# Performance work log

Hardware: AMD Instinct MI355X
Metric: run time of the kernel (lower is better)

## Reference

```python
import jax, jax.numpy as jnp
import numpy as np

N_NODES = 100000
D_IN = 128
D_OUT = 128
SHAPES = {"r1": 1, "r2": 2, "r3": 3}
N_EDGES = {"r1": 400000, "r2": 300000, "r3": 200000}


def setup_inputs() -> dict:
    key = jax.random.key(0)
    ks = jax.random.split(key, 10)
    inp = {
        "x": jax.random.normal(ks[0], (N_NODES, D_IN), dtype=jnp.float32),
        "A_r1": jax.random.normal(ks[1], (D_IN * 1, D_OUT), dtype=jnp.float32) * 0.05,
        "A_r2": jax.random.normal(ks[2], (D_IN * 2, D_OUT), dtype=jnp.float32) * 0.05,
        "A_r3": jax.random.normal(ks[3], (D_IN * 3, D_OUT), dtype=jnp.float32) * 0.05,
        "C_w": jax.random.normal(ks[4], (D_IN, D_OUT), dtype=jnp.float32) * 0.05,
        "C_b": jax.random.normal(ks[5], (D_OUT,), dtype=jnp.float32) * 0.05,
    }
    for j, (name, shape) in enumerate(SHAPES.items()):
        n = N_EDGES[name] * shape
        inp[f"ei_{name}"] = jax.random.randint(ks[6 + j], (2, n), 0, N_NODES, dtype=jnp.int64)
    return inp


def _edge_type_agg(x, edge_indices, A, shape):
    # edge_indices: [2, n_edges*shape]; row0 = sources, row1 reshaped -> dest per hyperedge
    dest = edge_indices[1].reshape(-1, shape)[:, 0]          # [n_edges]
    gathered = x[edge_indices[0]].reshape(-1, shape * x.shape[1])  # [n_edges, shape*D_IN]
    msg = gathered @ A                                        # [n_edges, D_OUT]
    # 1/count(dest) normalization (torch.unique counts == per-type in-degree)
    deg = jax.ops.segment_sum(jnp.ones_like(dest, dtype=msg.dtype), dest, num_segments=x.shape[0])
    msg = msg / deg[dest][:, None]
    return jax.ops.segment_sum(msg, dest, num_segments=x.shape[0])  # scatter_add


def reference(x, ei_r1, ei_r2, ei_r3, A_r1, A_r2, A_r3, C_w, C_b):
    agg = (_edge_type_agg(x, ei_r1, A_r1, 1)
           + _edge_type_agg(x, ei_r2, A_r2, 2)
           + _edge_type_agg(x, ei_r3, A_r3, 3))
    return x @ C_w + C_b + agg
```

## Files before the change

### kernel.cpp

```cpp
#include <hip/hip_runtime.h>

#define N_NODES 100000
#define D 128

typedef unsigned short u16;
typedef short s16x8 __attribute__((ext_vector_type(8)));
typedef float f32x4 __attribute__((ext_vector_type(4)));
typedef unsigned u32x4 __attribute__((ext_vector_type(4)));


#define ENTS_OFF 2804224L
#define AT_OFF   9204224L
#define XB_OFF   9433600L
#define G_OFF    35033600L

__device__ __forceinline__ u16 f2b(float f) {
    union { float f; unsigned u; } v; v.f = f;
    unsigned r = (v.u + 0x7FFFu + ((v.u >> 16) & 1u)) >> 16;
    return (u16)r;
}
__device__ __forceinline__ unsigned pk(float lo, float hi) {
    return (unsigned)f2b(lo) | ((unsigned)f2b(hi) << 16);
}
__device__ __forceinline__ float blo(unsigned w) { return __uint_as_float(w << 16); }
__device__ __forceinline__ float bhi(unsigned w) { return __uint_as_float(w & 0xFFFF0000u); }


__global__ __launch_bounds__(256) void deg_all(
    const int* __restrict__ e1, const int* __restrict__ e2, const int* __restrict__ e3,
    int ne1, int ne2, int ne3, int* __restrict__ deg) {
    int g = blockIdx.x * 256 + threadIdx.x;
    if (g < ne1) {
        atomicAdd(&deg[e1[ne1 + g]], 1);
    } else if (g < ne1 + ne2) {
        int e = g - ne1;
        atomicAdd(&deg[N_NODES + e2[ne2 * 2 + e * 2]], 1);
    } else if (g < ne1 + ne2 + ne3) {
        int e = g - ne1 - ne2;
        atomicAdd(&deg[2 * N_NODES + e3[ne3 * 3 + e * 3]], 1);
    }
}


__global__ __launch_bounds__(256) void scan_atb(
    const int* __restrict__ deg, int* __restrict__ offs, int* __restrict__ cursor,
    int* __restrict__ flags,
    const float* __restrict__ A1, const float* __restrict__ A2,
    const float* __restrict__ A3, const float* __restrict__ Cw,
    u16* __restrict__ ATb, int n, int nb) {
    const int t = threadIdx.x, bid = blockIdx.x;
    if (bid >= nb) {
        int mb = bid - nb;
        int m = mb >> 6;
        int idx = (mb & 63) * 256 + t;
        int nn = idx >> 7, kk = idx & 127;
        const float* src; int srow;
        if (m == 0)      { src = A1; srow = kk; }
        else if (m < 3)  { src = A2; srow = (m - 1) * 128 + kk; }
        else if (m < 6)  { src = A3; srow = (m - 3) * 128 + kk; }
        else             { src = Cw; srow = kk; }
        ATb[m * 16384 + nn * 128 + kk] = f2b(src[(long)srow * 128 + nn]);
        return;
    }
    __shared__ int s[256];
    __shared__ int bprefix;
    int base = bid * 1024 + t * 4;
    int d1[4], d2[4], v[4], p[4];
#pragma unroll
    for (int r = 0; r < 4; r++) {
        int idx = base + r;
        if (idx < n) {
            d1[r] = deg[idx];
            d2[r] = deg[N_NODES + idx];
            int d3 = deg[2 * N_NODES + idx];
            v[r] = d1[r] + 2 * d2[r] + 3 * d3;
        } else { d1[r] = 0; d2[r] = 0; v[r] = 0; }
    }
    p[0] = 0; p[1] = v[0]; p[2] = v[0] + v[1]; p[3] = v[0] + v[1] + v[2];
    int tsum = p[3] + v[3];
    s[t] = tsum;
    for (int off = 1; off < 256; off <<= 1) {
        __syncthreads();
        int x = (t >= off) ? s[t - off] : 0;
        __syncthreads();
        s[t] += x;
    }
    __syncthreads();
    int total = s[255];
    if (t == 0) {
        int run = 0;
        if (bid == 0) {
            atomicExch(&flags[0], (total << 2) | 2);
        } else {
            atomicExch(&flags[bid], (total << 2) | 1);
            int j = bid - 1;
            while (true) {
                int f = atomicAdd(&flags[j], 0);
                int st = f & 3;
                if (st == 0) continue;
                run += (f >> 2);
                if (st == 2) break;
                j--;
            }
            atomicExch(&flags[bid], ((run + total) << 2) | 2);
        }
        bprefix = run;
        if (bid == nb - 1) offs[n] = run + total;
    }
    __syncthreads();
    int texcl = s[t] - tsum + bprefix;
#pragma unroll
    for (int r = 0; r < 4; r++) {
        int idx = base + r;
        if (idx < n) {
            int val = texcl + p[r];
            offs[idx] = val;
            cursor[idx] = val;
            cursor[N_NODES + idx] = val + d1[r];
            cursor[2 * N_NODES + idx] = val + d1[r] + 2 * d2[r];
        }
    }
}


__global__ __launch_bounds__(256) void scatter_xconv(
    const float* __restrict__ x, u16* __restrict__ xb,
    const int* __restrict__ e1, const int* __restrict__ e2, const int* __restrict__ e3,
    int ne1, int ne2, int ne3, const int* __restrict__ deg,
    int* __restrict__ cursor, int* __restrict__ ents) {
    int b = blockIdx.x, t = threadIdx.x;
    if (b < 6250) {
        int f = b * 256 + t;
        int node = f >> 4, j = f & 15;
        const f32x4* xr = (const f32x4*)(x + (long)node * 128 + j * 8);
        f32x4 v0 = __builtin_nontemporal_load(xr);
        f32x4 v1 = __builtin_nontemporal_load(xr + 1);
        u32x4 o;
        o.x = pk(v0.x, v0.y); o.y = pk(v0.z, v0.w);
        o.z = pk(v1.x, v1.y); o.w = pk(v1.z, v1.w);
        *(u32x4*)(xb + (long)node * 128 + j * 8) = o;
        return;
    }
    int g = (b - 6250) * 256 + t;
    if (g < ne1) {
        int dest = e1[ne1 + g];
        int pos = atomicAdd(&cursor[dest], 1);
        ents[pos] = e1[g];
    } else if (g < ne1 + ne2) {
        int e = g - ne1;
        int dest = e2[ne2 * 2 + e * 2];
        int c2 = deg[N_NODES + dest];
        int pos = atomicAdd(&cursor[N_NODES + dest], 1);
        ents[pos]      = e2[e * 2];
        ents[pos + c2] = e2[e * 2 + 1];
    } else if (g < ne1 + ne2 + ne3) {
        int e = g - ne1 - ne2;
        int dest = e3[ne3 * 3 + e * 3];
        int c3 = deg[2 * N_NODES + dest];
        int pos = atomicAdd(&cursor[2 * N_NODES + dest], 1);
        ents[pos]          = e3[e * 3];
        ents[pos + c3]     = e3[e * 3 + 1];
        ents[pos + 2 * c3] = e3[e * 3 + 2];
    }
}


__global__ __launch_bounds__(256) void agg_all(
    const u16* __restrict__ xb, const int* __restrict__ ents,
    const int* __restrict__ offs, const int* __restrict__ deg,
    u16* __restrict__ G) {
    const int lane = threadIdx.x & 63;
    const int wv = __builtin_amdgcn_readfirstlane(threadIdx.x >> 6);
    int wid = blockIdx.x * 4 + wv;
    const int nw = gridDim.x * 4;
    const unsigned cb = (unsigned)lane * 4u;
    const char* xbb = (const char*)xb;

    for (int d = wid; d < N_NODES; d += nw) {
        const int lo = offs[d];
        const int c1 = deg[d], c2 = deg[N_NODES + d], c3 = deg[2 * N_NODES + d];
        float a0l = 0, a0h = 0, a1l = 0, a1h = 0, a2l = 0, a2h = 0;
        float a3l = 0, a3h = 0, a4l = 0, a4h = 0, a5l = 0, a5h = 0;

        int p = 0;
        for (; p + 8 <= c1; p += 8) {
            unsigned w[8];
#pragma unroll
            for (int i = 0; i < 8; i++)
                w[i] = *(const unsigned*)(xbb + (((unsigned)ents[lo + p + i] << 8) + cb));
#pragma unroll
            for (int i = 0; i < 8; i++) { a0l += blo(w[i]); a0h += bhi(w[i]); }
        }
        for (; p < c1; p++) {
            unsigned w = *(const unsigned*)(xbb + (((unsigned)ents[lo + p] << 8) + cb));
            a0l += blo(w); a0h += bhi(w);
        }

        const int o1 = lo + c1;
        p = 0;
        for (; p + 4 <= c2; p += 4) {
            unsigned wa[4], wb[4];
#pragma unroll
            for (int i = 0; i < 4; i++) {
                int e = o1 + p + i;
                wa[i] = *(const unsigned*)(xbb + (((unsigned)ents[e] << 8) + cb));
                wb[i] = *(const unsigned*)(xbb + (((unsigned)ents[e + c2] << 8) + cb));
            }
#pragma unroll
            for (int i = 0; i < 4; i++) {
                a1l += blo(wa[i]); a1h += bhi(wa[i]);
                a2l += blo(wb[i]); a2h += bhi(wb[i]);
            }
        }
        for (; p < c2; p++) {
            int e = o1 + p;
            unsigned wa = *(const unsigned*)(xbb + (((unsigned)ents[e] << 8) + cb));
            unsigned wb = *(const unsigned*)(xbb + (((unsigned)ents[e + c2] << 8) + cb));
            a1l += blo(wa); a1h += bhi(wa);
            a2l += blo(wb); a2h += bhi(wb);
        }

        const int o3 = o1 + 2 * c2;
        p = 0;
        for (; p + 4 <= c3; p += 4) {
            unsigned wa[4], wb[4], wc[4];
#pragma unroll
            for (int i = 0; i < 4; i++) {
                int e = o3 + p + i;
                wa[i] = *(const unsigned*)(xbb + (((unsigned)ents[e] << 8) + cb));
                wb[i] = *(const unsigned*)(xbb + (((unsigned)ents[e + c3] << 8) + cb));
                wc[i] = *(const unsigned*)(xbb + (((unsigned)ents[e + 2 * c3] << 8) + cb));
            }
#pragma unroll
            for (int i = 0; i < 4; i++) {
                a3l += blo(wa[i]); a3h += bhi(wa[i]);
                a4l += blo(wb[i]); a4h += bhi(wb[i]);
                a5l += blo(wc[i]); a5h += bhi(wc[i]);
            }
        }
        for (; p < c3; p++) {
            int e = o3 + p;
            unsigned wa = *(const unsigned*)(xbb + (((unsigned)ents[e] << 8) + cb));
            unsigned wb = *(const unsigned*)(xbb + (((unsigned)ents[e + c3] << 8) + cb));
            unsigned wc = *(const unsigned*)(xbb + (((unsigned)ents[e + 2 * c3] << 8) + cb));
            a3l += blo(wa); a3h += bhi(wa);
            a4l += blo(wb); a4h += bhi(wb);
            a5l += blo(wc); a5h += bhi(wc);
        }

        const float i1 = c1 ? 1.0f / (float)c1 : 0.0f;
        const float i2 = c2 ? 1.0f / (float)c2 : 0.0f;
        const float i3 = c3 ? 1.0f / (float)c3 : 0.0f;
        char* gd = (char*)G + (size_t)d * 1536 + cb;
        __builtin_nontemporal_store(pk(a0l * i1, a0h * i1), (unsigned*)gd);
        __builtin_nontemporal_store(pk(a1l * i2, a1h * i2), (unsigned*)(gd + 256));
        __builtin_nontemporal_store(pk(a2l * i2, a2h * i2), (unsigned*)(gd + 512));
        __builtin_nontemporal_store(pk(a3l * i3, a3h * i3), (unsigned*)(gd + 768));
        __builtin_nontemporal_store(pk(a4l * i3, a4h * i3), (unsigned*)(gd + 1024));
        __builtin_nontemporal_store(pk(a5l * i3, a5h * i3), (unsigned*)(gd + 1280));
    }
}


__global__ __launch_bounds__(256) void gemm_out(
    const u16* __restrict__ G, const u16* __restrict__ xb,
    const u16* __restrict__ AT, const float* __restrict__ Cb,
    float* __restrict__ out) {
    __shared__ __align__(16) u16 Xs[2][4][64][40];

    const int t = threadIdx.x;
    const int d0 = blockIdx.x * 64;
    const int lane = t & 63, wv = t >> 6;
    const int nbase = wv * 32, quad = lane >> 4, lrow = lane & 15;

    f32x4 acc[4][2];
#pragma unroll
    for (int mi = 0; mi < 4; mi++)
#pragma unroll
        for (int ni = 0; ni < 2; ni++) acc[mi][ni] = (f32x4)(0.0f);

    u32x4 stg[4];
#pragma unroll
    for (int i = 0; i < 4; i++) {
        int f = i * 256 + t;
        int row = f >> 4, k8 = f & 15;
        long rs = (d0 + row < N_NODES) ? d0 + row : N_NODES - 1;
        stg[i] = __builtin_nontemporal_load((const u32x4*)(G + rs * 768 + k8 * 8));
    }
#pragma unroll
    for (int i = 0; i < 4; i++) {
        int f = i * 256 + t;
        int row = f >> 4, k8 = f & 15;
        *(u32x4*)&Xs[0][k8 >> 2][row][(k8 & 3) * 8] = stg[i];
    }
    __syncthreads();

    for (int s = 0; s < 7; s++) {
        if (s < 6) {
#pragma unroll
            for (int i = 0; i < 4; i++) {
                int f = i * 256 + t;
                int row = f >> 4, k8 = f & 15;
                long rs = (d0 + row < N_NODES) ? d0 + row : N_NODES - 1;
                const u16* src = (s + 1 < 6) ? (G + rs * 768 + (s + 1) * 128 + k8 * 8)
                                             : (xb + rs * 128 + k8 * 8);
                stg[i] = __builtin_nontemporal_load((const u32x4*)src);
            }
        }
        const u16* B = AT + s * 16384;
        s16x8 bfrag[2][4];
#pragma unroll
        for (int ni = 0; ni < 2; ni++)
#pragma unroll
            for (int c = 0; c < 4; c++)
                bfrag[ni][c] = *(const s16x8*)(B + (nbase + ni * 16 + lrow) * 128 +
                                               c * 32 + quad * 8);
        const int cur = s & 1;
#pragma unroll
        for (int c = 0; c < 4; c++) {
            s16x8 a[4];
#pragma unroll
            for (int mi = 0; mi < 4; mi++)
                a[mi] = *(const s16x8*)&Xs[cur][c][mi * 16 + lrow][quad * 8];
#pragma unroll
            for (int mi = 0; mi < 4; mi++)
#pragma unroll
                for (int ni = 0; ni < 2; ni++)
                    acc[mi][ni] = __builtin_amdgcn_mfma_f32_16x16x32_bf16(
                        a[mi], bfrag[ni][c], acc[mi][ni], 0, 0, 0);
        }
        if (s < 6) {
#pragma unroll
            for (int i = 0; i < 4; i++) {
                int f = i * 256 + t;
                int row = f >> 4, k8 = f & 15;
                *(u32x4*)&Xs[cur ^ 1][k8 >> 2][row][(k8 & 3) * 8] = stg[i];
            }
        }
        __syncthreads();
    }

    float* smf = (float*)&Xs[0][0][0][0];
#pragma unroll
    for (int mi = 0; mi < 4; mi++)
#pragma unroll
        for (int ni = 0; ni < 2; ni++)
#pragma unroll
            for (int reg = 0; reg < 4; reg++) {
                int row = mi * 16 + quad * 4 + reg;
                int colq = nbase + ni * 16 + lrow;
                smf[row * 132 + colq] = acc[mi][ni][reg];
            }
    __syncthreads();
#pragma unroll
    for (int i = 0; i < 8; i++) {
        int f = i * 256 + t;
        int row = f >> 5;
        int colq = (f & 31) * 4;
        if (d0 + row < N_NODES) {
            f32x4 v = *(const f32x4*)&smf[row * 132 + colq];
            f32x4 b = *(const f32x4*)&Cb[colq];
            v += b;
            __builtin_nontemporal_store(v, (f32x4*)&out[(long)(d0 + row) * 128 + colq]);
        }
    }
}


extern "C" void kernel_launch(void* const* d_in, const int* in_sizes, int n_in,
                              void* d_out, int out_size, void* d_ws, size_t ws_size,
                              hipStream_t stream) {
    const float* x  = (const float*)d_in[0];
    const float* A1 = (const float*)d_in[1];
    const float* A2 = (const float*)d_in[2];
    const float* A3 = (const float*)d_in[3];
    const float* Cw = (const float*)d_in[4];
    const float* Cb = (const float*)d_in[5];
    const int* e1 = (const int*)d_in[6];
    const int* e2 = (const int*)d_in[7];
    const int* e3 = (const int*)d_in[8];
    float* out = (float*)d_out;

    int* ws = (int*)d_ws;
    int* deg    = ws;
    int* flags  = ws + 300000;
    int* offs   = ws + 300128;
    int* cursor = ws + 400129;
    int* ents   = (int*)((char*)d_ws + ENTS_OFF);
    u16* ATb    = (u16*)((char*)d_ws + AT_OFF);
    u16* xb     = (u16*)((char*)d_ws + XB_OFF);
    u16* G      = (u16*)((char*)d_ws + G_OFF);

    const int NE1 = in_sizes[6] / 2;
    const int NE2 = in_sizes[7] / (2 * 2);
    const int NE3 = in_sizes[8] / (2 * 3);
    const int NET = NE1 + NE2 + NE3;
    const int n = N_NODES;
    const int NB = (n + 1023) / 1024;

    hipMemsetAsync(deg, 0, (300000 + 128) * sizeof(int), stream);
    deg_all<<<(NET + 255) / 256, 256, 0, stream>>>(e1, e2, e3, NE1, NE2, NE3, deg);
    scan_atb<<<NB + 448, 256, 0, stream>>>(deg, offs, cursor, flags,
                                           A1, A2, A3, Cw, ATb, n, NB);
    scatter_xconv<<<6250 + (NET + 255) / 256, 256, 0, stream>>>(
        x, xb, e1, e2, e3, NE1, NE2, NE3, deg, cursor, ents);
    agg_all<<<2048, 256, 0, stream>>>(xb, ents, offs, deg, G);
    gemm_out<<<(N_NODES + 63) / 64, 256, 0, stream>>>(G, xb, ATb, Cb, out);
}
```

Measured before the change: 356.7 us.

## Process four destination nodes per wave in aggregation for more memory parallelism

The aggregation kernel now assigns four consecutive destination nodes to each wavefront and interleaves their gathers, looping to the maximum degree among the four with per-node predication. The aim is more independent gather loads in flight per wave, since degrees are small (about 4, 3 and 2 per type) and the old per-node loops had short trip counts and exposed latency. In exchange it adds predication overhead, wasted iterations when degrees differ, more registers, and fewer wave-level work items, which may hurt occupancy or load balance.

```diff
diff --git a/kernel.cpp b/kernel.cpp
--- a/kernel.cpp
+++ b/kernel.cpp
@@ -171,93 +171,134 @@
     u16* __restrict__ G) {
     const int lane = threadIdx.x & 63;
     const int wv = __builtin_amdgcn_readfirstlane(threadIdx.x >> 6);
-    int wid = blockIdx.x * 4 + wv;
+    const int wid = blockIdx.x * 4 + wv;
     const int nw = gridDim.x * 4;
     const unsigned cb = (unsigned)lane * 4u;
     const char* xbb = (const char*)xb;
-
-    for (int d = wid; d < N_NODES; d += nw) {
-        const int lo = offs[d];
-        const int c1 = deg[d], c2 = deg[N_NODES + d], c3 = deg[2 * N_NODES + d];
-        float a0l = 0, a0h = 0, a1l = 0, a1h = 0, a2l = 0, a2h = 0;
-        float a3l = 0, a3h = 0, a4l = 0, a4h = 0, a5l = 0, a5h = 0;
-
-        int p = 0;
-        for (; p + 8 <= c1; p += 8) {
-            unsigned w[8];
-#pragma unroll
-            for (int i = 0; i < 8; i++)
-                w[i] = *(const unsigned*)(xbb + (((unsigned)ents[lo + p + i] << 8) + cb));
-#pragma unroll
-            for (int i = 0; i < 8; i++) { a0l += blo(w[i]); a0h += bhi(w[i]); }
-        }
-        for (; p < c1; p++) {
-            unsigned w = *(const unsigned*)(xbb + (((unsigned)ents[lo + p] << 8) + cb));
-            a0l += blo(w); a0h += bhi(w);
-        }
-
-        const int o1 = lo + c1;
-        p = 0;
-        for (; p + 4 <= c2; p += 4) {
-            unsigned wa[4], wb[4];
-#pragma unroll
-            for (int i = 0; i < 4; i++) {
-                int e = o1 + p + i;
-                wa[i] = *(const unsigned*)(xbb + (((unsigned)ents[e] << 8) + cb));
-                wb[i] = *(const unsigned*)(xbb + (((unsigned)ents[e + c2] << 8) + cb));
-            }
-#pragma unroll
-            for (int i = 0; i < 4; i++) {
-                a1l += blo(wa[i]); a1h += bhi(wa[i]);
-                a2l += blo(wb[i]); a2h += bhi(wb[i]);
-            }
-        }
-        for (; p < c2; p++) {
-            int e = o1 + p;
-            unsigned wa = *(const unsigned*)(xbb + (((unsigned)ents[e] << 8) + cb));
-            unsigned wb = *(const unsigned*)(xbb + (((unsigned)ents[e + c2] << 8) + cb));
-            a1l += blo(wa); a1h += bhi(wa);
-            a2l += blo(wb); a2h += bhi(wb);
-        }
-
-        const int o3 = o1 + 2 * c2;
-        p = 0;
-        for (; p + 4 <= c3; p += 4) {
-            unsigned wa[4], wb[4], wc[4];
-#pragma unroll
-            for (int i = 0; i < 4; i++) {
-                int e = o3 + p + i;
-                wa[i] = *(const unsigned*)(xbb + (((unsigned)ents[e] << 8) + cb));
-                wb[i] = *(const unsigned*)(xbb + (((unsigned)ents[e + c3] << 8) + cb));
-                wc[i] = *(const unsigned*)(xbb + (((unsigned)ents[e + 2 * c3] << 8) + cb));
-            }
-#pragma unroll
-            for (int i = 0; i < 4; i++) {
-                a3l += blo(wa[i]); a3h += bhi(wa[i]);
-                a4l += blo(wb[i]); a4h += bhi(wb[i]);
-                a5l += blo(wc[i]); a5h += bhi(wc[i]);
-            }
-        }
-        for (; p < c3; p++) {
-            int e = o3 + p;
-            unsigned wa = *(const unsigned*)(xbb + (((unsigned)ents[e] << 8) + cb));
-            unsigned wb = *(const unsigned*)(xbb + (((unsigned)ents[e + c3] << 8) + cb));
-            unsigned wc = *(const unsigned*)(xbb + (((unsigned)ents[e + 2 * c3] << 8) + cb));
-            a3l += blo(wa); a3h += bhi(wa);
-            a4l += blo(wb); a4h += bhi(wb);
-            a5l += blo(wc); a5h += bhi(wc);
-        }
-
-        const float i1 = c1 ? 1.0f / (float)c1 : 0.0f;
-        const float i2 = c2 ? 1.0f / (float)c2 : 0.0f;
-        const float i3 = c3 ? 1.0f / (float)c3 : 0.0f;
-        char* gd = (char*)G + (size_t)d * 1536 + cb;
-        __builtin_nontemporal_store(pk(a0l * i1, a0h * i1), (unsigned*)gd);
-        __builtin_nontemporal_store(pk(a1l * i2, a1h * i2), (unsigned*)(gd + 256));
-        __builtin_nontemporal_store(pk(a2l * i2, a2h * i2), (unsigned*)(gd + 512));
-        __builtin_nontemporal_store(pk(a3l * i3, a3h * i3), (unsigned*)(gd + 768));
-        __builtin_nontemporal_store(pk(a4l * i3, a4h * i3), (unsigned*)(gd + 1024));
-        __builtin_nontemporal_store(pk(a5l * i3, a5h * i3), (unsigned*)(gd + 1280));
+    const int ngrp = N_NODES / 4;
+
+    for (int g = wid; g < ngrp; g += nw) {
+        const int d0 = g * 4;
+        int lo[4], c1[4], c2[4], c3[4];
+#pragma unroll
+        for (int j = 0; j < 4; j++) {
+            int d = d0 + j;
+            lo[j] = offs[d];
+            c1[j] = deg[d];
+            c2[j] = deg[N_NODES + d];
+            c3[j] = deg[2 * N_NODES + d];
+        }
+
+        float s0l[4], s0h[4];
+#pragma unroll
+        for (int j = 0; j < 4; j++) { s0l[j] = 0.0f; s0h[j] = 0.0f; }
+        {
+            int m = c1[0] > c1[1] ? c1[0] : c1[1];
+            int m2 = c1[2] > c1[3] ? c1[2] : c1[3];
+            if (m2 > m) m = m2;
+            for (int p = 0; p < m; p += 2) {
+                unsigned w[8];
+#pragma unroll
+                for (int j = 0; j < 4; j++) {
+                    if (p < c1[j])
+                        w[2 * j] = *(const unsigned*)(
+                            xbb + (((unsigned)ents[lo[j] + p] << 8) + cb));
+                    if (p + 1 < c1[j])
+                        w[2 * j + 1] = *(const unsigned*)(
+                            xbb + (((unsigned)ents[lo[j] + p + 1] << 8) + cb));
+                }
+#pragma unroll
+                for (int j = 0; j < 4; j++) {
+                    if (p < c1[j])     { s0l[j] += blo(w[2 * j]);     s0h[j] += bhi(w[2 * j]); }
+                    if (p + 1 < c1[j]) { s0l[j] += blo(w[2 * j + 1]); s0h[j] += bhi(w[2 * j + 1]); }
+                }
+            }
+        }
+#pragma unroll
+        for (int j = 0; j < 4; j++) {
+            float inv = c1[j] ? 1.0f / (float)c1[j] : 0.0f;
+            __builtin_nontemporal_store(
+                pk(s0l[j] * inv, s0h[j] * inv),
+                (unsigned*)((char*)G + (size_t)(d0 + j) * 1536 + cb));
+        }
+
+        float s1l[4], s1h[4], s2l[4], s2h[4];
+#pragma unroll
+        for (int j = 0; j < 4; j++) { s1l[j] = 0; s1h[j] = 0; s2l[j] = 0; s2h[j] = 0; }
+        {
+            int m = c2[0] > c2[1] ? c2[0] : c2[1];
+            int m2 = c2[2] > c2[3] ? c2[2] : c2[3];
+            if (m2 > m) m = m2;
+            for (int p = 0; p < m; p++) {
+                unsigned wa[4], wb[4];
+#pragma unroll
+                for (int j = 0; j < 4; j++) {
+                    if (p < c2[j]) {
+                        int e = lo[j] + c1[j] + p;
+                        wa[j] = *(const unsigned*)(
+                            xbb + (((unsigned)ents[e] << 8) + cb));
+                        wb[j] = *(const unsigned*)(
+                            xbb + (((unsigned)ents[e + c2[j]] << 8) + cb));
+                    }
+                }
+#pragma unroll
+                for (int j = 0; j < 4; j++) {
+                    if (p < c2[j]) {
+                        s1l[j] += blo(wa[j]); s1h[j] += bhi(wa[j]);
+                        s2l[j] += blo(wb[j]); s2h[j] += bhi(wb[j]);
+                    }
+                }
+            }
+        }
+#pragma unroll
+        for (int j = 0; j < 4; j++) {
+            float inv = c2[j] ? 1.0f / (float)c2[j] : 0.0f;
+            char* gd = (char*)G + (size_t)(d0 + j) * 1536 + cb;
+            __builtin_nontemporal_store(pk(s1l[j] * inv, s1h[j] * inv), (unsigned*)(gd + 256));
+            __builtin_nontemporal_store(pk(s2l[j] * inv, s2h[j] * inv), (unsigned*)(gd + 512));
+        }
+
+        float t3l[4], t3h[4], t4l[4], t4h[4], t5l[4], t5h[4];
+#pragma unroll
+        for (int j = 0; j < 4; j++) {
+            t3l[j] = 0; t3h[j] = 0; t4l[j] = 0; t4h[j] = 0; t5l[j] = 0; t5h[j] = 0;
+        }
+        {
+            int m = c3[0] > c3[1] ? c3[0] : c3[1];
+            int m2 = c3[2] > c3[3] ? c3[2] : c3[3];
+            if (m2 > m) m = m2;
+            for (int p = 0; p < m; p++) {
+                unsigned wa[4], wb[4], wc[4];
+#pragma unroll
+                for (int j = 0; j < 4; j++) {
+                    if (p < c3[j]) {
+                        int e = lo[j] + c1[j] + 2 * c2[j] + p;
+                        wa[j] = *(const unsigned*)(
+                            xbb + (((unsigned)ents[e] << 8) + cb));
+                        wb[j] = *(const unsigned*)(
+                            xbb + (((unsigned)ents[e + c3[j]] << 8) + cb));
+                        wc[j] = *(const unsigned*)(
+                            xbb + (((unsigned)ents[e + 2 * c3[j]] << 8) + cb));
+                    }
+                }
+#pragma unroll
+                for (int j = 0; j < 4; j++) {
+                    if (p < c3[j]) {
+                        t3l[j] += blo(wa[j]); t3h[j] += bhi(wa[j]);
+                        t4l[j] += blo(wb[j]); t4h[j] += bhi(wb[j]);
+                        t5l[j] += blo(wc[j]); t5h[j] += bhi(wc[j]);
+                    }
+                }
+            }
+        }
+#pragma unroll
+        for (int j = 0; j < 4; j++) {
+            float inv = c3[j] ? 1.0f / (float)c3[j] : 0.0f;
+            char* gd = (char*)G + (size_t)(d0 + j) * 1536 + cb;
+            __builtin_nontemporal_store(pk(t3l[j] * inv, t3h[j] * inv), (unsigned*)(gd + 768));
+            __builtin_nontemporal_store(pk(t4l[j] * inv, t4h[j] * inv), (unsigned*)(gd + 1024));
+            __builtin_nontemporal_store(pk(t5l[j] * inv, t5h[j] * inv), (unsigned*)(gd + 1280));
+        }
     }
 }
 
```

Result: slower. 387.1 us (+8.5%).
